# Kernel optimization log

Measured on AMD Instinct MI355X. Metric: run time of the kernel, lower is better.

Reference implementation:

```python
import jax, jax.numpy as jnp
import numpy as np

N, NFEAT, K, HK = 500000, 64, 8, 64

def _trunc_normal(key, shape, std):
    # torch.nn.init.trunc_normal_ truncates at +/-2 (then scaled by std)
    return jnp.clip(jax.random.normal(key, shape), -2.0, 2.0) * std

def setup_inputs() -> dict:
    key = jax.random.key(0)
    kx, kz, kt = jax.random.split(key, 3)
    x = jax.random.normal(kx, (N, NFEAT), dtype=jnp.float32)
    # stacked ParameterList: z[i] in R^{h_K x n}, t[i] in R^{h_K}
    z = _trunc_normal(kz, (K, HK, NFEAT), 1.0).astype(jnp.float32)  # b_z = 1.0
    t = _trunc_normal(kt, (K, HK), 1.0).astype(jnp.float32)         # b_t = 1.0
    return {"x": x, "z": z, "t": t}

def reference(x, z, t):
    w = jnp.exp(z)                                  # [K, HK, n], positive weights
    g = jnp.einsum('ni,khi->nkh', x, w) + t         # [N, K, HK]
    max_vals = jnp.max(g, axis=2)                   # [N, K] maxout per group
    max_idx = jnp.argmax(g, axis=2)                 # [N, K]
    y = jnp.min(max_vals, axis=1)                   # [N]   min over groups
    min_idx = jnp.argmin(max_vals, axis=1)          # [N]
    # A[min_idx[n], max_idx[n, min_idx[n]]] += 1  (vectorized scatter-add)
    cols = jnp.take_along_axis(max_idx, min_idx[:, None], axis=1)[:, 0]  # [N]
    A = jnp.zeros((K, HK), dtype=jnp.float32).at[min_idx, cols].add(1.0)
    return y, A
```

## Files before the change

kernel.cpp:

```cpp
#include <hip/hip_runtime.h>
#include <math.h>

constexpr int NS    = 500000;
constexpr int NF    = 64;
constexpr int KG    = 8;
constexpr int HKC   = 64;
constexpr int NCELL = KG * HKC;
constexpr int RPW   = 32;
constexpr int RPB   = 128;
constexpr int NBLK  = (NS + RPB - 1) / RPB;
constexpr int NSLOT = 1954;
constexpr int SLICE = HKC * NF;

typedef __attribute__((ext_vector_type(8))) _Float16 half8;
typedef __attribute__((ext_vector_type(4))) float f32x4;

__device__ __forceinline__ float swz16_f(float v) {
    return __int_as_float(__builtin_amdgcn_ds_swizzle(__float_as_int(v), 0x401F));
}
__device__ __forceinline__ int swz16_i(int v) {
    return __builtin_amdgcn_ds_swizzle(v, 0x401F);
}

__global__ void prep_kernel(const float* __restrict__ z,
                            _Float16* __restrict__ w_hi,
                            _Float16* __restrict__ w_lo,
                            float* __restrict__ A,
                            float4* __restrict__ pzero, int n4) {
    int i = blockIdx.x * blockDim.x + threadIdx.x;
    if (i < KG * HKC * NF) {
        float w = expf(z[i]);
        _Float16 h = (_Float16)w;
        w_hi[i] = h;
        w_lo[i] = (_Float16)(w - (float)h);
    }
    if (i < NCELL) A[i] = 0.0f;
    for (int j = i; j < n4; j += gridDim.x * blockDim.x)
        pzero[j] = (float4){0.f, 0.f, 0.f, 0.f};
}

template <bool PRIV>
__global__ __launch_bounds__(256, 3) void monn_mfma_kernel(
    const float* __restrict__ x,
    const _Float16* __restrict__ w_hi,
    const _Float16* __restrict__ w_lo,
    const float* __restrict__ t,
    float* __restrict__ y,
    float* __restrict__ dest) {

    __shared__ __align__(16) char smem[2 * 8192];
    __shared__ unsigned lhist[NCELL];
    if (PRIV) {
        for (int i = threadIdx.x; i < NCELL; i += 256) lhist[i] = 0u;
    }

    const int tid  = threadIdx.x;
    const int lane = tid & 63;
    const long base  = (long)blockIdx.x * RPB + (tid >> 6) * RPW;
    const bool valid = (base < NS);
    const long cbase = valid ? base : (NS - RPW);
    const int m  = lane & 15;
    const int q  = lane >> 4;
    const int q4 = q * 4;
    const int a32 = ((lane ^ 32) << 2);
    const int x7  = m & 7;
    const int rb0 = m * 128 + (((0 + q) ^ x7) << 4);
    const int rb1 = m * 128 + (((4 + q) ^ x7) << 4);
    const int sr  = tid >> 2;
    const int sc  = (tid & 3) * 2;
    const int sd0 = sr * 128 + (((sc)     ^ (sr & 7)) << 4);
    const int sd1 = sr * 128 + (((sc + 1) ^ (sr & 7)) << 4);

    half8 Xh[2][2], Xl[2][2];
#pragma unroll
    for (int rt = 0; rt < 2; ++rt) {
        const float* xp = x + (cbase + rt * 16 + m) * NF;
#pragma unroll
        for (int s = 0; s < 2; ++s) {
            const int k0 = s * 32 + q * 8;
            const float4 v0 = *reinterpret_cast<const float4*>(xp + k0);
            const float4 v1 = *reinterpret_cast<const float4*>(xp + k0 + 4);
            const float f[8] = {v0.x, v0.y, v0.z, v0.w, v1.x, v1.y, v1.z, v1.w};
#pragma unroll
            for (int j = 0; j < 8; ++j) {
                _Float16 h = (_Float16)f[j];
                Xh[rt][s][j] = h;
                Xl[rt][s][j] = (_Float16)(f[j] - (float)h);
            }
        }
    }

    float ymin[2] = {INFINITY, INFINITY};
    int   code[2] = {0, 0};

#pragma unroll 1
    for (int g = 0; g < KG; ++g) {
        __syncthreads();
        {
            const float4* sh = reinterpret_cast<const float4*>(w_hi + (size_t)g * SLICE);
            const float4* sl = reinterpret_cast<const float4*>(w_lo + (size_t)g * SLICE);
            const float4 h0 = sh[tid * 2], h1 = sh[tid * 2 + 1];
            const float4 l0 = sl[tid * 2], l1 = sl[tid * 2 + 1];
            *reinterpret_cast<float4*>(smem + sd0)        = h0;
            *reinterpret_cast<float4*>(smem + sd1)        = h1;
            *reinterpret_cast<float4*>(smem + 8192 + sd0) = l0;
            *reinterpret_cast<float4*>(smem + 8192 + sd1) = l1;
        }
        __syncthreads();

        f32x4 acc[4][2];
#pragma unroll
        for (int c = 0; c < 4; ++c) {
            const float4 tv = *reinterpret_cast<const float4*>(t + g * HKC + c * 16 + q4);
            const f32x4 tin = (f32x4){tv.x, tv.y, tv.z, tv.w};
            acc[c][0] = tin;
            acc[c][1] = tin;
        }

#pragma unroll
        for (int s = 0; s < 2; ++s) {
            const int rb = s ? rb1 : rb0;
            half8 Wh[4], Wl[4];
#pragma unroll
            for (int c = 0; c < 4; ++c) {
                Wh[c] = *reinterpret_cast<const half8*>(smem + rb + c * 2048);
                Wl[c] = *reinterpret_cast<const half8*>(smem + 8192 + rb + c * 2048);
            }
#pragma unroll
            for (int c = 0; c < 4; ++c)
#pragma unroll
                for (int rt = 0; rt < 2; ++rt)
                    acc[c][rt] = __builtin_amdgcn_mfma_f32_16x16x32_f16(Wh[c], Xh[rt][s], acc[c][rt], 0, 0, 0);
#pragma unroll
            for (int c = 0; c < 4; ++c)
#pragma unroll
                for (int rt = 0; rt < 2; ++rt)
                    acc[c][rt] = __builtin_amdgcn_mfma_f32_16x16x32_f16(Wl[c], Xh[rt][s], acc[c][rt], 0, 0, 0);
#pragma unroll
            for (int c = 0; c < 4; ++c)
#pragma unroll
                for (int rt = 0; rt < 2; ++rt)
                    acc[c][rt] = __builtin_amdgcn_mfma_f32_16x16x32_f16(Wh[c], Xl[rt][s], acc[c][rt], 0, 0, 0);
        }

#pragma unroll
        for (int rt = 0; rt < 2; ++rt) {
            float t01 = fmaxf(acc[0][rt][0], acc[0][rt][1]);
            float t23 = fmaxf(acc[0][rt][2], acc[0][rt][3]);
            float t45 = fmaxf(acc[1][rt][0], acc[1][rt][1]);
            float t67 = fmaxf(acc[1][rt][2], acc[1][rt][3]);
            float t89 = fmaxf(acc[2][rt][0], acc[2][rt][1]);
            float tab = fmaxf(acc[2][rt][2], acc[2][rt][3]);
            float tcd = fmaxf(acc[3][rt][0], acc[3][rt][1]);
            float tef = fmaxf(acc[3][rt][2], acc[3][rt][3]);
            float v = fmaxf(fmaxf(fmaxf(t01, t23), fmaxf(t45, t67)),
                            fmaxf(fmaxf(t89, tab), fmaxf(tcd, tef)));
            int h = 0;
#pragma unroll
            for (int c = 3; c >= 0; --c)
#pragma unroll
                for (int j = 3; j >= 0; --j)
                    h = (acc[c][rt][j] == v) ? (c * 16 + j) : h;
            h |= q4;
            {
                float v2 = swz16_f(v);
                int   h2 = swz16_i(h);
                bool take = (v2 > v) || (v2 == v && h2 < h);
                v = take ? v2 : v;  h = take ? h2 : h;
                float v3 = __int_as_float(__builtin_amdgcn_ds_bpermute(a32, __float_as_int(v)));
                int   h3 = __builtin_amdgcn_ds_bpermute(a32, h);
                take = (v3 > v) || (v3 == v && h3 < h);
                v = take ? v3 : v;  h = take ? h3 : h;
            }
            const bool better = v < ymin[rt];
            ymin[rt] = fminf(ymin[rt], v);
            code[rt] = better ? ((g << 6) | h) : code[rt];
        }
    }

    if (valid && q == 0) {
#pragma unroll
        for (int rt = 0; rt < 2; ++rt) {
            y[base + rt * 16 + m] = ymin[rt];
            if (PRIV) atomicAdd(&lhist[code[rt]], 1u);
            else      atomicAdd(&dest[code[rt]], 1.0f);
        }
    }

    if (PRIV) {
        __syncthreads();
        float* p = dest + (size_t)(blockIdx.x >> 1) * NCELL;
        for (int i = threadIdx.x; i < NCELL; i += 256) {
            const unsigned c = lhist[i];
            if (c) atomicAdd(&p[i], (float)c);
        }
    }
}

__global__ void reduce_kernel(const float* __restrict__ partial, float* __restrict__ A) {
    const int tid = blockIdx.x * blockDim.x + threadIdx.x;
    const int c = tid & (NCELL - 1);
    const int s = tid >> 9;
    float sum = 0.0f;
    for (int b = s; b < NSLOT; b += 32)
        sum += partial[(size_t)b * NCELL + c];
    atomicAdd(&A[c], sum);
}

extern "C" void kernel_launch(void* const* d_in, const int* in_sizes, int n_in,
                              void* d_out, int out_size, void* d_ws, size_t ws_size,
                              hipStream_t stream) {
    const float* x = (const float*)d_in[0];
    const float* z = (const float*)d_in[1];
    const float* t = (const float*)d_in[2];

    float* y = (float*)d_out;
    float* A = (float*)d_out + NS;

    _Float16* w_hi = (_Float16*)d_ws;
    _Float16* w_lo = w_hi + (size_t)KG * HKC * NF;
    float* partial = (float*)((char*)d_ws + 2 * sizeof(_Float16) * KG * HKC * NF);

    const size_t need = 2 * sizeof(_Float16) * KG * HKC * NF
                      + (size_t)NSLOT * NCELL * sizeof(float);

    const bool priv = (ws_size >= need);
    const int n4 = priv ? (NSLOT * NCELL / 4) : 0;

    prep_kernel<<<1024, 256, 0, stream>>>(z, w_hi, w_lo, A, (float4*)partial, n4);

    if (priv) {
        monn_mfma_kernel<true><<<NBLK, 256, 0, stream>>>(x, w_hi, w_lo, t, y, partial);
        reduce_kernel<<<64, 256, 0, stream>>>(partial, A);
    } else {
        monn_mfma_kernel<false><<<NBLK, 256, 0, stream>>>(x, w_hi, w_lo, t, y, A);
    }
}
```

Before: 267.0 us.

## Double-buffer weight slices in LDS, defer cross-lane reductions, shrink partial histogram slots

Stages the next group's weight slice in registers and writes it into a second LDS buffer while the current group runs its MFMAs, cutting one barrier per group and overlapping global loads with compute. The per-group cross-lane max reductions are deferred to after the loop and batched, and the group loop is fully unrolled. The private histogram slot count drops from 1954 to 64 (blocks map by modulo), which shrinks the zero-fill and the reduce pass but raises atomic contention per slot. Shared memory doubles and register pressure grows, which may lower occupancy under the launch bound of 3.

New measurement: 500.8 us. 1.88x slower.

```diff
diff --git a/kernel.cpp b/kernel.cpp
--- a/kernel.cpp
+++ b/kernel.cpp
@@ -9,7 +9,7 @@
 constexpr int RPW   = 32;
 constexpr int RPB   = 128;
 constexpr int NBLK  = (NS + RPB - 1) / RPB;
-constexpr int NSLOT = 1954;
+constexpr int NSLOT = 64;
 constexpr int SLICE = HKC * NF;
 
 typedef __attribute__((ext_vector_type(8))) _Float16 half8;
@@ -35,8 +35,7 @@
         w_lo[i] = (_Float16)(w - (float)h);
     }
     if (i < NCELL) A[i] = 0.0f;
-    for (int j = i; j < n4; j += gridDim.x * blockDim.x)
-        pzero[j] = (float4){0.f, 0.f, 0.f, 0.f};
+    if (i < n4) pzero[i] = (float4){0.f, 0.f, 0.f, 0.f};
 }
 
 template <bool PRIV>
@@ -48,7 +47,7 @@
     float* __restrict__ y,
     float* __restrict__ dest) {
 
-    __shared__ __align__(16) char smem[2 * 8192];
+    __shared__ __align__(16) char smem[2 * 16384];
     __shared__ unsigned lhist[NCELL];
     if (PRIV) {
         for (int i = threadIdx.x; i < NCELL; i += 256) lhist[i] = 0u;
@@ -90,23 +89,32 @@
         }
     }
 
-    float ymin[2] = {INFINITY, INFINITY};
-    int   code[2] = {0, 0};
-
-#pragma unroll 1
+    float4 ph0, ph1, pl0, pl1;
+    {
+        const float4* sh = reinterpret_cast<const float4*>(w_hi);
+        const float4* sl = reinterpret_cast<const float4*>(w_lo);
+        ph0 = sh[tid * 2]; ph1 = sh[tid * 2 + 1];
+        pl0 = sl[tid * 2]; pl1 = sl[tid * 2 + 1];
+    }
+    *reinterpret_cast<float4*>(smem + sd0)        = ph0;
+    *reinterpret_cast<float4*>(smem + sd1)        = ph1;
+    *reinterpret_cast<float4*>(smem + 8192 + sd0) = pl0;
+    *reinterpret_cast<float4*>(smem + 8192 + sd1) = pl1;
+    __syncthreads();
+
+    float vmx[2][8];
+    int   hmx[2][8];
+
+#pragma unroll
     for (int g = 0; g < KG; ++g) {
-        __syncthreads();
-        {
-            const float4* sh = reinterpret_cast<const float4*>(w_hi + (size_t)g * SLICE);
-            const float4* sl = reinterpret_cast<const float4*>(w_lo + (size_t)g * SLICE);
-            const float4 h0 = sh[tid * 2], h1 = sh[tid * 2 + 1];
-            const float4 l0 = sl[tid * 2], l1 = sl[tid * 2 + 1];
-            *reinterpret_cast<float4*>(smem + sd0)        = h0;
-            *reinterpret_cast<float4*>(smem + sd1)        = h1;
-            *reinterpret_cast<float4*>(smem + 8192 + sd0) = l0;
-            *reinterpret_cast<float4*>(smem + 8192 + sd1) = l1;
-        }
-        __syncthreads();
+        const int bufo = (g & 1) * 16384;
+
+        if (g < KG - 1) {
+            const float4* sh = reinterpret_cast<const float4*>(w_hi + (size_t)(g + 1) * SLICE);
+            const float4* sl = reinterpret_cast<const float4*>(w_lo + (size_t)(g + 1) * SLICE);
+            ph0 = sh[tid * 2]; ph1 = sh[tid * 2 + 1];
+            pl0 = sl[tid * 2]; pl1 = sl[tid * 2 + 1];
+        }
 
         f32x4 acc[4][2];
 #pragma unroll
@@ -119,7 +127,7 @@
 
 #pragma unroll
         for (int s = 0; s < 2; ++s) {
-            const int rb = s ? rb1 : rb0;
+            const int rb = bufo + (s ? rb1 : rb0);
             half8 Wh[4], Wl[4];
 #pragma unroll
             for (int c = 0; c < 4; ++c) {
@@ -161,8 +169,29 @@
 #pragma unroll
                 for (int j = 3; j >= 0; --j)
                     h = (acc[c][rt][j] == v) ? (c * 16 + j) : h;
-            h |= q4;
-            {
+            vmx[rt][g] = v;
+            hmx[rt][g] = h | q4;
+        }
+
+        if (g < KG - 1) {
+            const int obuf = 16384 - bufo;
+            *reinterpret_cast<float4*>(smem + obuf + sd0)        = ph0;
+            *reinterpret_cast<float4*>(smem + obuf + sd1)        = ph1;
+            *reinterpret_cast<float4*>(smem + obuf + 8192 + sd0) = pl0;
+            *reinterpret_cast<float4*>(smem + obuf + 8192 + sd1) = pl1;
+            __syncthreads();
+        }
+    }
+
+    if (valid) {
+#pragma unroll
+        for (int rt = 0; rt < 2; ++rt) {
+            float vc[8];
+            int   hc[8];
+#pragma unroll
+            for (int g = 0; g < KG; ++g) {
+                float v = vmx[rt][g];
+                int   h = hmx[rt][g];
                 float v2 = swz16_f(v);
                 int   h2 = swz16_i(h);
                 bool take = (v2 > v) || (v2 == v && h2 < h);
@@ -170,26 +199,28 @@
                 float v3 = __int_as_float(__builtin_amdgcn_ds_bpermute(a32, __float_as_int(v)));
                 int   h3 = __builtin_amdgcn_ds_bpermute(a32, h);
                 take = (v3 > v) || (v3 == v && h3 < h);
-                v = take ? v3 : v;  h = take ? h3 : h;
-            }
-            const bool better = v < ymin[rt];
-            ymin[rt] = fminf(ymin[rt], v);
-            code[rt] = better ? ((g << 6) | h) : code[rt];
-        }
-    }
-
-    if (valid && q == 0) {
-#pragma unroll
-        for (int rt = 0; rt < 2; ++rt) {
-            y[base + rt * 16 + m] = ymin[rt];
-            if (PRIV) atomicAdd(&lhist[code[rt]], 1u);
-            else      atomicAdd(&dest[code[rt]], 1.0f);
+                vc[g] = take ? v3 : v;
+                hc[g] = take ? h3 : h;
+            }
+            float ymin = vc[0];
+            int   code = hc[0];
+#pragma unroll
+            for (int g = 1; g < KG; ++g) {
+                const bool better = vc[g] < ymin;
+                ymin = fminf(ymin, vc[g]);
+                code = better ? ((g << 6) | hc[g]) : code;
+            }
+            if (q == 0) {
+                y[base + rt * 16 + m] = ymin;
+                if (PRIV) atomicAdd(&lhist[code], 1u);
+                else      atomicAdd(&dest[code], 1.0f);
+            }
         }
     }
 
     if (PRIV) {
         __syncthreads();
-        float* p = dest + (size_t)(blockIdx.x >> 1) * NCELL;
+        float* p = dest + (size_t)(blockIdx.x & (NSLOT - 1)) * NCELL;
         for (int i = threadIdx.x; i < NCELL; i += 256) {
             const unsigned c = lhist[i];
             if (c) atomicAdd(&p[i], (float)c);
@@ -227,7 +258,7 @@
     const bool priv = (ws_size >= need);
     const int n4 = priv ? (NSLOT * NCELL / 4) : 0;
 
-    prep_kernel<<<1024, 256, 0, stream>>>(z, w_hi, w_lo, A, (float4*)partial, n4);
+    prep_kernel<<<128, 256, 0, stream>>>(z, w_hi, w_lo, A, (float4*)partial, n4);
 
     if (priv) {
         monn_mfma_kernel<true><<<NBLK, 256, 0, stream>>>(x, w_hi, w_lo, t, y, partial);
```
